# Kernel tuning notes

Hardware: AMD Instinct MI355X
Metric: run time of the kernel (lower is better)

The kernel has to match this reference:

```python
import jax, jax.numpy as jnp
import numpy as np

# module hyperparams (init_kwargs)
IN_SIZE = 64      # D
OUT_SIZE = 64     # D_
NUM_CLUSTER = 8   # K
HEADS = 4         # H
GAMMA = 1.0
TAU = 10.0

E = 400000        # num edges
N_NODES = 50000


def setup_inputs() -> dict:
    key = jax.random.key(0)
    ks = jax.random.split(key, 8)
    msg = jax.random.normal(ks[0], (E, OUT_SIZE), dtype=jnp.float32)
    x_i = jax.random.normal(ks[1], (E, IN_SIZE), dtype=jnp.float32)
    x_j = jax.random.normal(ks[2], (E, IN_SIZE), dtype=jnp.float32)
    e_ij = jax.random.normal(ks[3], (E, IN_SIZE), dtype=jnp.float32)
    index = jax.random.randint(ks[4], (E,), 0, N_NODES, dtype=jnp.int32)
    # xavier-uniform-ish cluster centers [H, K, D]
    lim = float(np.sqrt(6.0 / (NUM_CLUSTER + IN_SIZE)))
    k = jax.random.uniform(ks[5], (HEADS, NUM_CLUSTER, IN_SIZE), dtype=jnp.float32,
                           minval=-lim, maxval=lim)
    # final Linear(K*D_ -> D_), stored as [in, out]
    limw = float(np.sqrt(1.0 / (NUM_CLUSTER * OUT_SIZE)))
    W = jax.random.uniform(ks[6], (NUM_CLUSTER * OUT_SIZE, OUT_SIZE), dtype=jnp.float32,
                           minval=-limw, maxval=limw)
    b = jax.random.uniform(ks[7], (OUT_SIZE,), dtype=jnp.float32, minval=-limw, maxval=limw)
    return {"msg": msg, "x_i": x_i, "x_j": x_j, "e_ij": e_ij, "index": index,
            "num_nodes": N_NODES, "k": k, "W": W, "b": b}


def reference(msg, x_i, x_j, e_ij, index, num_nodes, k, W, b):
    H, K, D, D_ = HEADS, NUM_CLUSTER, IN_SIZE, OUT_SIZE
    # agg_q = elementwise sum of neighbor features and edge features -> [E, D]
    x = x_j + e_ij
    kf = k.reshape(H * K, D)
    # squared euclidean distances: [H*K, E]
    dist = (jnp.sum(kf * kf, axis=1)[:, None]
            + jnp.sum(x * x, axis=1)[None, :]
            - 2.0 * (kf @ x.T))
    dist = jnp.maximum(dist, 0.0)
    # Student-t kernel
    t = (1.0 + dist / GAMMA) ** (-(GAMMA + 1.0) / 2.0)
    t = t.reshape(H, K, -1).transpose(2, 1, 0)  # [E, K, H]
    w = t / jnp.sum(t, axis=1, keepdims=True) * TAU  # normalize over clusters
    w = jax.nn.softmax(jnp.mean(w, axis=-1), axis=-1)  # [E, K]
    # weight messages per cluster -> [E, K*D_]
    new_msg = (w[:, :, None] * msg[:, None, :]).reshape(-1, K * D_)
    agg = jax.ops.segment_sum(new_msg, index, num_segments=num_nodes)  # [N, K*D_]
    out = agg @ W + b
    return jax.nn.leaky_relu(out, negative_slope=0.01)
```

## Files before the change

### kernel.cpp

```cpp
#include <hip/hip_runtime.h>
#include <hip/hip_bf16.h>

typedef unsigned short u16;
typedef unsigned int   u32;
typedef unsigned long long u64;

typedef __attribute__((ext_vector_type(8))) short  short8;
typedef __attribute__((ext_vector_type(4))) float  floatx4;

#define FIX_SCALE 65536.0f
#define FIX_INV   (1.0f / 65536.0f)
#define FIX_BIAS  (1 << 26)

__device__ __forceinline__ u32 rne_pack(float lo, float hi) {
  u32 bl = __float_as_uint(lo), bh = __float_as_uint(hi);
  u32 rl = ((bl + 0x7FFFu + ((bl >> 16) & 1u)) >> 16) & 0xFFFFu;
  u32 rh = (bh + 0x7FFFu + ((bh >> 16) & 1u)) & 0xFFFF0000u;
  return rl | rh;
}

__device__ __forceinline__ short8 scale_frag(uint4 mraw, float w) {
  const u32* in = (const u32*)&mraw;
  uint4 o; u32* ou = (u32*)&o;
  #pragma unroll
  for (int i = 0; i < 4; ++i) {
    float lo = __uint_as_float(in[i] << 16) * w;
    float hi = __uint_as_float(in[i]) * w;
    ou[i] = __builtin_amdgcn_perm(__float_as_uint(hi), __float_as_uint(lo), 0x07060302u);
  }
  return *(short8*)&o;
}

__global__ __launch_bounds__(256, 2) void fused_kernel(
    const float* __restrict__ msg, const float* __restrict__ xj,
    const float* __restrict__ eij, const float* __restrict__ kc,
    const float* __restrict__ Wg, const int* __restrict__ idx,
    u64* __restrict__ o64, int E) {
  __shared__ __align__(16) char un[65536];
  float* tl = (float*)un;
  u16*   Wl = (u16*)un;
  __shared__ __align__(16) float wsm[2048];
  __shared__ float kn[32];

  const int tid  = threadIdx.x;
  const int lane = tid & 63, wv = tid >> 6;
  const int ln   = lane & 15, q  = lane >> 4;
  const int e0   = blockIdx.x * 256;

  const float4* kc4 = (const float4*)kc;
  short8 af[2][2];
  float knp[2] = {0.f, 0.f};
  #pragma unroll
  for (int mt = 0; mt < 2; ++mt) {
    #pragma unroll
    for (int kk = 0; kk < 2; ++kk) {
      size_t b4 = (size_t)(mt * 16 + ln) * 16 + kk * 8 + q * 2;
      float4 c0 = kc4[b4], c1 = kc4[b4 + 1];
      knp[mt] += c0.x*c0.x + c0.y*c0.y + c0.z*c0.z + c0.w*c0.w
               + c1.x*c1.x + c1.y*c1.y + c1.z*c1.z + c1.w*c1.w;
      u32 pk[4] = { rne_pack(c0.x, c0.y), rne_pack(c0.z, c0.w),
                    rne_pack(c1.x, c1.y), rne_pack(c1.z, c1.w) };
      af[mt][kk] = *(short8*)pk;
    }
    float s = knp[mt];
    s += __shfl_xor(s, 16);
    s += __shfl_xor(s, 32);
    if (wv == 0 && q == 0) kn[mt * 16 + ln] = s;
  }

  const float4* xj4  = (const float4*)xj;
  const float4* eij4 = (const float4*)eij;
  #pragma unroll
  for (int g = 0; g < 4; ++g) {
    int el = wv * 64 + g * 16 + ln;
    int ge = e0 + el; if (ge >= E) ge = 0;
    size_t b4 = (size_t)ge * 16 + q * 2;
    float4 x0 = xj4[b4],     x1 = xj4[b4 + 1];
    float4 x2 = xj4[b4 + 8], x3 = xj4[b4 + 9];
    float4 ea0 = eij4[b4],     ea1 = eij4[b4 + 1];
    float4 ea2 = eij4[b4 + 8], ea3 = eij4[b4 + 9];
    float s0x = x0.x+ea0.x, s0y = x0.y+ea0.y, s0z = x0.z+ea0.z, s0w = x0.w+ea0.w;
    float s1x = x1.x+ea1.x, s1y = x1.y+ea1.y, s1z = x1.z+ea1.z, s1w = x1.w+ea1.w;
    float s2x = x2.x+ea2.x, s2y = x2.y+ea2.y, s2z = x2.z+ea2.z, s2w = x2.w+ea2.w;
    float s3x = x3.x+ea3.x, s3y = x3.y+ea3.y, s3z = x3.z+ea3.z, s3w = x3.w+ea3.w;
    float ps = s0x*s0x + s0y*s0y + s0z*s0z + s0w*s0w
             + s1x*s1x + s1y*s1y + s1z*s1z + s1w*s1w
             + s2x*s2x + s2y*s2y + s2z*s2z + s2w*s2w
             + s3x*s3x + s3y*s3y + s3z*s3z + s3w*s3w;
    u32 p0[4] = { rne_pack(s0x, s0y), rne_pack(s0z, s0w),
                  rne_pack(s1x, s1y), rne_pack(s1z, s1w) };
    u32 p1[4] = { rne_pack(s2x, s2y), rne_pack(s2z, s2w),
                  rne_pack(s3x, s3y), rne_pack(s3z, s3w) };
    ps += __shfl_xor(ps, 16);
    ps += __shfl_xor(ps, 32);
    short8 bb0 = *(short8*)p0, bb1 = *(short8*)p1;
    floatx4 acc0 = {0.f,0.f,0.f,0.f}, acc1 = {0.f,0.f,0.f,0.f};
    acc0 = __builtin_amdgcn_mfma_f32_16x16x32_bf16(af[0][0], bb0, acc0, 0, 0, 0);
    acc0 = __builtin_amdgcn_mfma_f32_16x16x32_bf16(af[0][1], bb1, acc0, 0, 0, 0);
    acc1 = __builtin_amdgcn_mfma_f32_16x16x32_bf16(af[1][0], bb0, acc1, 0, 0, 0);
    acc1 = __builtin_amdgcn_mfma_f32_16x16x32_bf16(af[1][1], bb1, acc1, 0, 0, 0);
    #pragma unroll
    for (int i = 0; i < 4; ++i) {
      tl[el * 33 + (q * 4 + i)]      = acc0[i];
      tl[el * 33 + 16 + (q * 4 + i)] = acc1[i];
    }
    if (q == 0) tl[el * 33 + 32] = ps;
  }
  __syncthreads();

  {
    int e = tid;
    bool valid = (e0 + e) < E;
    float xn = tl[e * 33 + 32];
    float tv[32];
    float hs[4] = {0.f, 0.f, 0.f, 0.f};
    #pragma unroll
    for (int c = 0; c < 32; ++c) {
      float dist = kn[c] + xn - 2.f * tl[e * 33 + c];
      dist = dist > 0.f ? dist : 0.f;
      float t = 1.f / (1.f + dist);
      tv[c] = t;
      hs[c >> 3] += t;
    }
    float r0 = 1.f / hs[0], r1 = 1.f / hs[1], r2 = 1.f / hs[2], r3 = 1.f / hs[3];
    float m[8], mx = -1e30f;
    #pragma unroll
    for (int k = 0; k < 8; ++k) {
      m[k] = 2.5f * (tv[k] * r0 + tv[8 + k] * r1 + tv[16 + k] * r2 + tv[24 + k] * r3);
      mx = m[k] > mx ? m[k] : mx;
    }
    float p[8], sum = 0.f;
    #pragma unroll
    for (int k = 0; k < 8; ++k) { p[k] = __expf(m[k] - mx); sum += p[k]; }
    float rs = valid ? (1.f / sum) : 0.f;
    floatx4 w0 = {p[0]*rs, p[1]*rs, p[2]*rs, p[3]*rs};
    floatx4 w1 = {p[4]*rs, p[5]*rs, p[6]*rs, p[7]*rs};
    *(floatx4*)&wsm[e * 8]     = w0;
    *(floatx4*)&wsm[e * 8 + 4] = w1;
  }
  __syncthreads();

  #pragma unroll
  for (int it = 0; it < 16; ++it) {
    int c  = (tid >> 6) + it * 4;
    int kk = c >> 2, q2 = c & 3, n = tid & 63;
    const float* src = Wg + (size_t)(kk * 32 + q2 * 8) * 64 + n;
    u32 pk[4];
    #pragma unroll
    for (int jp = 0; jp < 4; ++jp)
      pk[jp] = rne_pack(src[(jp * 2) * 64], src[(jp * 2 + 1) * 64]);
    int tt = (n & 1) + ((n >> 5) << 1);
    int mm = tt * 16 + ((n & 31) >> 1);
    *(uint4*)&Wl[(c * 64 + mm) * 8] = *(uint4*)pk;
  }

  const float4* msg4 = (const float4*)msg;
  uint4 mf[4][2];
  const int edgebase = e0 + wv * 64;
  #pragma unroll
  for (int s = 0; s < 4; ++s) {
    int eg = edgebase + s * 16 + ln; if (eg >= E) eg = E - 1;
    size_t mb = (size_t)eg * 16 + q * 2;
    #pragma unroll
    for (int h = 0; h < 2; ++h) {
      float4 m0 = msg4[mb + h * 8], m1 = msg4[mb + h * 8 + 1];
      u32 pk[4] = { rne_pack(m0.x, m0.y), rne_pack(m0.z, m0.w),
                    rne_pack(m1.x, m1.y), rne_pack(m1.z, m1.w) };
      mf[s][h] = *(uint4*)pk;
    }
  }
  floatx4 wf[4][2];
  #pragma unroll
  for (int s = 0; s < 4; ++s) {
    int eL = wv * 64 + s * 16 + ln;
    wf[s][0] = *(floatx4*)&wsm[eL * 8];
    wf[s][1] = *(floatx4*)&wsm[eL * 8 + 4];
  }
  floatx4 acc[4][4];
  #pragma unroll
  for (int s = 0; s < 4; ++s)
    #pragma unroll
    for (int t = 0; t < 4; ++t) { floatx4 z = {0.f,0.f,0.f,0.f}; acc[s][t] = z; }
  __syncthreads();

  #pragma unroll
  for (int kb = 0; kb < 8; ++kb) {
    float wsc[4];
    #pragma unroll
    for (int s = 0; s < 4; ++s) wsc[s] = wf[s][kb >> 2][kb & 3];
    #pragma unroll
    for (int hh = 0; hh < 2; ++hh) {
      int kk = kb * 2 + hh;
      short8 bfr[4];
      #pragma unroll
      for (int t = 0; t < 4; ++t)
        bfr[t] = *(short8*)&Wl[((kk * 4 + q) * 64 + t * 16 + ln) * 8];
      #pragma unroll
      for (int s = 0; s < 4; ++s) {
        short8 a = scale_frag(mf[s][hh], wsc[s]);
        #pragma unroll
        for (int t = 0; t < 4; ++t)
          acc[s][t] = __builtin_amdgcn_mfma_f32_16x16x32_bf16(a, bfr[t], acc[s][t], 0, 0, 0);
      }
    }
  }

  #pragma unroll
  for (int s = 0; s < 4; ++s) {
    #pragma unroll
    for (int i = 0; i < 4; ++i) {
      int eg = edgebase + s * 16 + q * 4 + i;
      if (eg < E) {
        int node = idx[eg];
        u64* dst = o64 + (size_t)node * 32 + ln;
        u32 l0 = (u32)((int)rintf(acc[s][0][i] * FIX_SCALE) + FIX_BIAS);
        u32 h0 = (u32)((int)rintf(acc[s][1][i] * FIX_SCALE) + FIX_BIAS);
        u32 l1 = (u32)((int)rintf(acc[s][2][i] * FIX_SCALE) + FIX_BIAS);
        u32 h1 = (u32)((int)rintf(acc[s][3][i] * FIX_SCALE) + FIX_BIAS);
        atomicAdd(dst,      ((u64)h0 << 32) | l0);
        atomicAdd(dst + 16, ((u64)h1 << 32) | l1);
      }
    }
  }
}

__global__ __launch_bounds__(256) void finish_packed(
    u64* __restrict__ a64, const float* __restrict__ b, int ng) {
  int g = blockIdx.x * 256 + threadIdx.x;
  if (g >= ng) return;
  int node = g >> 3, pg = g & 7;
  u64* ap = a64 + (size_t)node * 32 + pg * 4;
  ulonglong4 v = *(ulonglong4*)ap;
  u32 w[8] = { (u32)v.x, (u32)(v.x >> 32), (u32)v.y, (u32)(v.y >> 32),
               (u32)v.z, (u32)(v.z >> 32), (u32)v.w, (u32)(v.w >> 32) };
  u32 cnt = (w[0] + (1u << 25)) >> 26;
  u32 cb  = cnt << 26;
  int col0 = pg * 8;
  float r[8];
  #pragma unroll
  for (int c = 0; c < 8; ++c) {
    float z = (float)(int)(w[c] - cb) * FIX_INV + b[col0 + c];
    r[c] = z > 0.f ? z : 0.01f * z;
  }
  float* op = (float*)a64 + (size_t)node * 64 + col0;
  *(float4*)op       = make_float4(r[0], r[1], r[2], r[3]);
  *(float4*)(op + 4) = make_float4(r[4], r[5], r[6], r[7]);
}

extern "C" void kernel_launch(void* const* d_in, const int* in_sizes, int n_in,
                              void* d_out, int out_size, void* d_ws, size_t ws_size,
                              hipStream_t stream) {
  const float* msg = (const float*)d_in[0];
  const float* xj  = (const float*)d_in[2];
  const float* eij = (const float*)d_in[3];
  const int*   idx = (const int*)d_in[4];
  const float* kc  = (const float*)d_in[6];
  const float* Wg  = (const float*)d_in[7];
  const float* bg  = (const float*)d_in[8];

  int E    = in_sizes[0] / 64;
  int Nout = out_size;
  float* out = (float*)d_out;

  hipMemsetAsync(out, 0, (size_t)Nout * 4, stream);

  int blocks = (E + 255) / 256;
  fused_kernel<<<blocks, 256, 0, stream>>>(msg, xj, eij, kc, Wg, idx,
                                           (u64*)out, E);

  int ng = Nout / 8;
  finish_packed<<<(ng + 255) / 256, 256, 0, stream>>>((u64*)out, bg, ng);
}
```

Baseline: 408.1 us.

## Double block size to 512 threads and pack LDS intermediates as fp16

Each block now handles 512 edges with 512 threads. The per-edge distance partials (cluster norm minus twice the dot product) and the softmax cluster weights are stored in shared memory as packed fp16 instead of fp32, which halves their LDS footprint so the larger block fits in the same 64KB union. The per-cluster norms move from an LDS array to register shuffles, and the W staging loop is halved because twice as many threads share it. Precision drops for the distance terms and weights, and launch bounds of 512 threads with 4 blocks per CU limit registers per thread, which may cause spills.

```diff
diff --git a/kernel.cpp b/kernel.cpp
--- a/kernel.cpp
+++ b/kernel.cpp
@@ -7,6 +7,7 @@
 
 typedef __attribute__((ext_vector_type(8))) short  short8;
 typedef __attribute__((ext_vector_type(4))) float  floatx4;
+typedef __attribute__((ext_vector_type(2))) __fp16 half2v;
 
 #define FIX_SCALE 65536.0f
 #define FIX_INV   (1.0f / 65536.0f)
@@ -19,6 +20,15 @@
   return rl | rh;
 }
 
+__device__ __forceinline__ u32 pk_f16(float lo, float hi) {
+  half2v h = __builtin_amdgcn_cvt_pkrtz(lo, hi);
+  return *(u32*)&h;
+}
+__device__ __forceinline__ float2 unpk_f16(u32 v) {
+  half2v h = *(half2v*)&v;
+  return make_float2((float)h.x, (float)h.y);
+}
+
 __device__ __forceinline__ short8 scale_frag(uint4 mraw, float w) {
   const u32* in = (const u32*)&mraw;
   uint4 o; u32* ou = (u32*)&o;
@@ -31,41 +41,46 @@
   return *(short8*)&o;
 }
 
-__global__ __launch_bounds__(256, 2) void fused_kernel(
+__global__ __launch_bounds__(512, 4) void fused_kernel(
     const float* __restrict__ msg, const float* __restrict__ xj,
     const float* __restrict__ eij, const float* __restrict__ kc,
     const float* __restrict__ Wg, const int* __restrict__ idx,
     u64* __restrict__ o64, int E) {
   __shared__ __align__(16) char un[65536];
-  float* tl = (float*)un;
+  u32*   tl = (u32*)un;
   u16*   Wl = (u16*)un;
-  __shared__ __align__(16) float wsm[2048];
-  __shared__ float kn[32];
+  __shared__ __align__(16) u32 wsm[2048];
 
   const int tid  = threadIdx.x;
   const int lane = tid & 63, wv = tid >> 6;
   const int ln   = lane & 15, q  = lane >> 4;
-  const int e0   = blockIdx.x * 256;
+  const int e0   = blockIdx.x * 512;
 
   const float4* kc4 = (const float4*)kc;
   short8 af[2][2];
-  float knp[2] = {0.f, 0.f};
+  float knr[2];
   #pragma unroll
   for (int mt = 0; mt < 2; ++mt) {
+    float knp = 0.f;
     #pragma unroll
     for (int kk = 0; kk < 2; ++kk) {
       size_t b4 = (size_t)(mt * 16 + ln) * 16 + kk * 8 + q * 2;
       float4 c0 = kc4[b4], c1 = kc4[b4 + 1];
-      knp[mt] += c0.x*c0.x + c0.y*c0.y + c0.z*c0.z + c0.w*c0.w
-               + c1.x*c1.x + c1.y*c1.y + c1.z*c1.z + c1.w*c1.w;
+      knp += c0.x*c0.x + c0.y*c0.y + c0.z*c0.z + c0.w*c0.w
+           + c1.x*c1.x + c1.y*c1.y + c1.z*c1.z + c1.w*c1.w;
       u32 pk[4] = { rne_pack(c0.x, c0.y), rne_pack(c0.z, c0.w),
                     rne_pack(c1.x, c1.y), rne_pack(c1.z, c1.w) };
       af[mt][kk] = *(short8*)pk;
     }
-    float s = knp[mt];
-    s += __shfl_xor(s, 16);
-    s += __shfl_xor(s, 32);
-    if (wv == 0 && q == 0) kn[mt * 16 + ln] = s;
+    knp += __shfl_xor(knp, 16);
+    knp += __shfl_xor(knp, 32);
+    knr[mt] = knp;
+  }
+  float kni0[4], kni1[4];
+  #pragma unroll
+  for (int i = 0; i < 4; ++i) {
+    kni0[i] = __shfl(knr[0], q * 4 + i);
+    kni1[i] = __shfl(knr[1], q * 4 + i);
   }
 
   const float4* xj4  = (const float4*)xj;
@@ -100,27 +115,31 @@
     acc1 = __builtin_amdgcn_mfma_f32_16x16x32_bf16(af[1][0], bb0, acc1, 0, 0, 0);
     acc1 = __builtin_amdgcn_mfma_f32_16x16x32_bf16(af[1][1], bb1, acc1, 0, 0, 0);
     #pragma unroll
-    for (int i = 0; i < 4; ++i) {
-      tl[el * 33 + (q * 4 + i)]      = acc0[i];
-      tl[el * 33 + 16 + (q * 4 + i)] = acc1[i];
-    }
-    if (q == 0) tl[el * 33 + 32] = ps;
+    for (int j = 0; j < 2; ++j) {
+      tl[el * 17 + q * 2 + j] =
+          pk_f16(kni0[2*j] - 2.f * acc0[2*j], kni0[2*j+1] - 2.f * acc0[2*j+1]);
+      tl[el * 17 + 8 + q * 2 + j] =
+          pk_f16(kni1[2*j] - 2.f * acc1[2*j], kni1[2*j+1] - 2.f * acc1[2*j+1]);
+    }
+    if (q == 0) tl[el * 17 + 16] = __float_as_uint(ps);
   }
   __syncthreads();
 
   {
     int e = tid;
     bool valid = (e0 + e) < E;
-    float xn = tl[e * 33 + 32];
+    float xn = __uint_as_float(tl[e * 17 + 16]);
     float tv[32];
     float hs[4] = {0.f, 0.f, 0.f, 0.f};
     #pragma unroll
-    for (int c = 0; c < 32; ++c) {
-      float dist = kn[c] + xn - 2.f * tl[e * 33 + c];
-      dist = dist > 0.f ? dist : 0.f;
-      float t = 1.f / (1.f + dist);
-      tv[c] = t;
-      hs[c >> 3] += t;
+    for (int p = 0; p < 16; ++p) {
+      float2 d2 = unpk_f16(tl[e * 17 + p]);
+      float dist0 = xn + d2.x; dist0 = dist0 > 0.f ? dist0 : 0.f;
+      float dist1 = xn + d2.y; dist1 = dist1 > 0.f ? dist1 : 0.f;
+      float t0 = 1.f / (1.f + dist0);
+      float t1 = 1.f / (1.f + dist1);
+      tv[2*p] = t0; tv[2*p+1] = t1;
+      hs[p >> 2] += t0 + t1;
     }
     float r0 = 1.f / hs[0], r1 = 1.f / hs[1], r2 = 1.f / hs[2], r3 = 1.f / hs[3];
     float m[8], mx = -1e30f;
@@ -133,16 +152,15 @@
     #pragma unroll
     for (int k = 0; k < 8; ++k) { p[k] = __expf(m[k] - mx); sum += p[k]; }
     float rs = valid ? (1.f / sum) : 0.f;
-    floatx4 w0 = {p[0]*rs, p[1]*rs, p[2]*rs, p[3]*rs};
-    floatx4 w1 = {p[4]*rs, p[5]*rs, p[6]*rs, p[7]*rs};
-    *(floatx4*)&wsm[e * 8]     = w0;
-    *(floatx4*)&wsm[e * 8 + 4] = w1;
+    uint4 wpk = { pk_f16(p[0]*rs, p[1]*rs), pk_f16(p[2]*rs, p[3]*rs),
+                  pk_f16(p[4]*rs, p[5]*rs), pk_f16(p[6]*rs, p[7]*rs) };
+    *(uint4*)&wsm[e * 4] = wpk;
   }
   __syncthreads();
 
   #pragma unroll
-  for (int it = 0; it < 16; ++it) {
-    int c  = (tid >> 6) + it * 4;
+  for (int it = 0; it < 8; ++it) {
+    int c  = (tid >> 6) + it * 8;
     int kk = c >> 2, q2 = c & 3, n = tid & 63;
     const float* src = Wg + (size_t)(kk * 32 + q2 * 8) * 64 + n;
     u32 pk[4];
@@ -169,12 +187,11 @@
       mf[s][h] = *(uint4*)pk;
     }
   }
-  floatx4 wf[4][2];
+  uint4 wf[4];
   #pragma unroll
   for (int s = 0; s < 4; ++s) {
     int eL = wv * 64 + s * 16 + ln;
-    wf[s][0] = *(floatx4*)&wsm[eL * 8];
-    wf[s][1] = *(floatx4*)&wsm[eL * 8 + 4];
+    wf[s] = *(uint4*)&wsm[eL * 4];
   }
   floatx4 acc[4][4];
   #pragma unroll
@@ -187,7 +204,11 @@
   for (int kb = 0; kb < 8; ++kb) {
     float wsc[4];
     #pragma unroll
-    for (int s = 0; s < 4; ++s) wsc[s] = wf[s][kb >> 2][kb & 3];
+    for (int s = 0; s < 4; ++s) {
+      u32 wd = ((const u32*)&wf[s])[kb >> 1];
+      half2v hv = *(half2v*)&wd;
+      wsc[s] = (kb & 1) ? (float)hv.y : (float)hv.x;
+    }
     #pragma unroll
     for (int hh = 0; hh < 2; ++hh) {
       int kk = kb * 2 + hh;
@@ -262,10 +283,10 @@
   int Nout = out_size;
   float* out = (float*)d_out;
 
-  hipMemsetAsync(out, 0, (size_t)Nout * 4, stream);
-
-  int blocks = (E + 255) / 256;
-  fused_kernel<<<blocks, 256, 0, stream>>>(msg, xj, eij, kc, Wg, idx,
+  (void)hipMemsetAsync(out, 0, (size_t)Nout * 4, stream);
+
+  int blocks = (E + 511) / 512;
+  fused_kernel<<<blocks, 512, 0, stream>>>(msg, xj, eij, kc, Wg, idx,
                                            (u64*)out, E);
 
   int ng = Nout / 8;
```

New measurement: 602.0 us. 1.48x slower.
